# Performance work log

Measured on AMD Instinct MI355X. Metric: run time of the kernel, lower is better.

Reference implementation:

```python
import jax, jax.numpy as jnp
import numpy as np

B, N1, N2, D = 2, 500, 800, 128
THRESHOLD = 0.5

def setup_inputs() -> dict:
    key = jax.random.key(0)
    ks = jax.random.split(key, 7)
    return {
        "S_mol1": jax.random.randint(ks[0], (B, N1), 0, 21),
        "S_mol2": jax.random.randint(ks[1], (B, N2), 0, 21),
        "h_mol1": jax.random.normal(ks[2], (B, N1, D), jnp.float32),
        "h_mol2": jax.random.normal(ks[3], (B, N2, D), jnp.float32),
        "contact_map": jax.random.uniform(ks[4], (B, N1, N2), jnp.float32),
        "W1": jax.random.normal(ks[5], (2 * D, D), jnp.float32) / np.sqrt(2 * D).astype(np.float32),
        "b1": jnp.zeros((D,), jnp.float32),
        "W2": jax.random.normal(ks[6], (D, 1), jnp.float32) / np.sqrt(D).astype(np.float32),
        "b2": jnp.zeros((1,), jnp.float32),
    }

def reference(S_mol1, S_mol2, h_mol1, h_mol2, contact_map, W1, b1, W2, b2):
    m1 = (S_mol1 != 0).astype(jnp.float32)  # [B,N1]
    m2 = (S_mol2 != 0).astype(jnp.float32)  # [B,N2]
    # cat([h1_expand, h2_expand]) @ W1 == h1 @ W1[:D] + h2 @ W1[D:], broadcast over pairs
    p1 = jnp.einsum('bnd,df->bnf', h_mol1, W1[:D])   # [B,N1,D]
    p2 = jnp.einsum('bmd,df->bmf', h_mol2, W1[D:])   # [B,N2,D]
    hidden = jax.nn.relu(p1[:, :, None, :] + p2[:, None, :, :] + b1)  # [B,N1,N2,D]
    pred = (jnp.einsum('bnmd,do->bnmo', hidden, W2) + b2)[..., 0]     # [B,N1,N2]
    mask = m1[:, :, None] * m2[:, None, :]                             # [B,N1,N2]
    y_contact = (contact_map < THRESHOLD).astype(jnp.float32) * mask
    return (pred.reshape(B, -1), y_contact.reshape(B, -1), mask.reshape(B, -1))
```

## Files before the change

kernel.cpp:

```cpp
#include <hip/hip_runtime.h>

#define D_  128
#define B_  2
#define N1_ 500
#define N2_ 800

__global__ __launch_bounds__(256) void proj_kernel(
    const float* __restrict__ h1, const float* __restrict__ h2,
    const float* __restrict__ W1, const float* __restrict__ b1,
    float* __restrict__ P1, float* __restrict__ P2)
{
    __shared__ float hs[8][128];
    const int NB1 = (B_ * N1_ + 7) / 8;
    bool isP1 = (int)blockIdx.x < NB1;
    int r0 = (isP1 ? (int)blockIdx.x : (int)blockIdx.x - NB1) * 8;
    int R  = isP1 ? B_ * N1_ : B_ * N2_;
    const float* __restrict__ src = isP1 ? h1 : h2;
    float* __restrict__ dst = isP1 ? P1 : P2;
    const int koff = isP1 ? 0 : D_;

    int tid = threadIdx.x;
    {
        int row = tid >> 5;
        int c4  = (tid & 31) * 4;
        float4 v = make_float4(0.f, 0.f, 0.f, 0.f);
        int r = r0 + row;
        if (r < R) v = *reinterpret_cast<const float4*>(&src[(size_t)r * D_ + c4]);
        *reinterpret_cast<float4*>(&hs[row][c4]) = v;
    }
    __syncthreads();

    int c  = tid & 127;
    int rg = tid >> 7;
    const float* __restrict__ Wc = W1 + (size_t)koff * D_ + c;
    float acc[4];
    float binit = isP1 ? b1[c] : 0.f;
    #pragma unroll
    for (int i = 0; i < 4; ++i) acc[i] = binit;

    #pragma unroll 4
    for (int k4 = 0; k4 < D_; k4 += 4) {
        float w0 = Wc[(k4 + 0) * D_];
        float w1 = Wc[(k4 + 1) * D_];
        float w2 = Wc[(k4 + 2) * D_];
        float w3 = Wc[(k4 + 3) * D_];
        #pragma unroll
        for (int i = 0; i < 4; ++i) {
            float4 h = *reinterpret_cast<const float4*>(&hs[rg * 4 + i][k4]);
            acc[i] = fmaf(h.x, w0, acc[i]);
            acc[i] = fmaf(h.y, w1, acc[i]);
            acc[i] = fmaf(h.z, w2, acc[i]);
            acc[i] = fmaf(h.w, w3, acc[i]);
        }
    }
    #pragma unroll
    for (int i = 0; i < 4; ++i) {
        int r = r0 + rg * 4 + i;
        if (r < R) dst[(size_t)r * D_ + c] = acc[i];
    }
}

__global__ __launch_bounds__(256) void pair_kernel(
    const int* __restrict__ S1, const int* __restrict__ S2,
    const float* __restrict__ contact,
    const float* __restrict__ P1, const float* __restrict__ P2,
    const float* __restrict__ W2, const float* __restrict__ b2,
    float* __restrict__ out)
{
    const int NT = 16, MT = 128;
    const int nTn = (N1_ + NT - 1) / NT;
    const int nTm = (N2_ + MT - 1) / MT;
    int bid = blockIdx.x;
    int tb  = bid / (nTn * nTm);
    int rem = bid % (nTn * nTm);
    int tn  = rem / nTm;
    int tm  = rem % nTm;
    int n0 = tn * NT, m0 = tm * MT;
    int tid = threadIdx.x, lane = tid & 63, wave = tid >> 6;
    bool fullTile = (m0 + MT <= N2_);

    __shared__ float p2s[128 * 132];
    __shared__ float p1s[16 * 128];
    __shared__ float w2s[128];
    __shared__ float m1s[16];

    const float* __restrict__ P2b = P2 + ((size_t)tb * N2_ + m0) * D_;
    #pragma unroll
    for (int j = 0; j < 16; ++j) {
        int fi  = tid + j * 256;
        int row = fi >> 5;
        int c4  = (fi & 31) * 4;
        float4 v = make_float4(0.f, 0.f, 0.f, 0.f);
        if (m0 + row < N2_) v = *reinterpret_cast<const float4*>(&P2b[row * D_ + c4]);
        *reinterpret_cast<float4*>(&p2s[row * 132 + c4]) = v;
    }
    const float* __restrict__ P1b = P1 + ((size_t)tb * N1_ + n0) * D_;
    #pragma unroll
    for (int j = 0; j < 2; ++j) {
        int fi  = tid + j * 256;
        int row = fi >> 5;
        int c4  = (fi & 31) * 4;
        float4 v = make_float4(0.f, 0.f, 0.f, 0.f);
        if (n0 + row < N1_) v = *reinterpret_cast<const float4*>(&P1b[row * D_ + c4]);
        *reinterpret_cast<float4*>(&p1s[row * 128 + c4]) = v;
    }
    if (tid < 32)
        *reinterpret_cast<float4*>(&w2s[tid * 4]) =
            *reinterpret_cast<const float4*>(&W2[tid * 4]);
    if (tid >= 64 && tid < 80) {
        int i = tid - 64;
        m1s[i] = (n0 + i < N1_ && S1[tb * N1_ + n0 + i] != 0) ? 1.f : 0.f;
    }
    int mA = m0 + lane;
    int mB = m0 + 64 + lane;
    float m2A = (mA < N2_ && S2[tb * N2_ + mA] != 0) ? 1.f : 0.f;
    float m2B = (fullTile && S2[tb * N2_ + mB] != 0) ? 1.f : 0.f;
    float bias2 = b2[0];
    __syncthreads();

    int nw = wave * 4;
    float acc0[4] = {0.f, 0.f, 0.f, 0.f};
    float acc1[4] = {0.f, 0.f, 0.f, 0.f};
    const float* p2a = &p2s[lane * 132];
    const float* p2b = &p2s[(lane + 64) * 132];
    const float* p1p = &p1s[nw * 128];

    if (fullTile) {
        #pragma unroll 4
        for (int d = 0; d < D_; d += 4) {
            float4 qa = *reinterpret_cast<const float4*>(&p2a[d]);
            float4 qb = *reinterpret_cast<const float4*>(&p2b[d]);
            float4 w  = *reinterpret_cast<const float4*>(&w2s[d]);
            #pragma unroll
            for (int i = 0; i < 4; ++i) {
                float4 q1 = *reinterpret_cast<const float4*>(&p1p[i * 128 + d]);
                acc0[i] = fmaf(fmaxf(q1.x + qa.x, 0.f), w.x, acc0[i]);
                acc0[i] = fmaf(fmaxf(q1.y + qa.y, 0.f), w.y, acc0[i]);
                acc0[i] = fmaf(fmaxf(q1.z + qa.z, 0.f), w.z, acc0[i]);
                acc0[i] = fmaf(fmaxf(q1.w + qa.w, 0.f), w.w, acc0[i]);
                acc1[i] = fmaf(fmaxf(q1.x + qb.x, 0.f), w.x, acc1[i]);
                acc1[i] = fmaf(fmaxf(q1.y + qb.y, 0.f), w.y, acc1[i]);
                acc1[i] = fmaf(fmaxf(q1.z + qb.z, 0.f), w.z, acc1[i]);
                acc1[i] = fmaf(fmaxf(q1.w + qb.w, 0.f), w.w, acc1[i]);
            }
        }
    } else {
        #pragma unroll 4
        for (int d = 0; d < D_; d += 4) {
            float4 qa = *reinterpret_cast<const float4*>(&p2a[d]);
            float4 w  = *reinterpret_cast<const float4*>(&w2s[d]);
            #pragma unroll
            for (int i = 0; i < 4; ++i) {
                float4 q1 = *reinterpret_cast<const float4*>(&p1p[i * 128 + d]);
                acc0[i] = fmaf(fmaxf(q1.x + qa.x, 0.f), w.x, acc0[i]);
                acc0[i] = fmaf(fmaxf(q1.y + qa.y, 0.f), w.y, acc0[i]);
                acc0[i] = fmaf(fmaxf(q1.z + qa.z, 0.f), w.z, acc0[i]);
                acc0[i] = fmaf(fmaxf(q1.w + qa.w, 0.f), w.w, acc0[i]);
            }
        }
    }

    const size_t NN  = (size_t)N1_ * N2_;
    const size_t TOT = (size_t)B_ * NN;
    #pragma unroll
    for (int i = 0; i < 4; ++i) {
        int n = n0 + nw + i;
        if (n >= N1_) break;
        float m1v = m1s[nw + i];
        size_t rowoff = (size_t)tb * NN + (size_t)n * N2_;
        if (mA < N2_) {
            float mk = m1v * m2A;
            size_t off = rowoff + mA;
            float cv = contact[off];
            out[off]           = acc0[i] + bias2;
            out[TOT + off]     = (cv < 0.5f) ? mk : 0.f;
            out[2 * TOT + off] = mk;
        }
        if (fullTile) {
            float mk = m1v * m2B;
            size_t off = rowoff + mB;
            float cv = contact[off];
            out[off]           = acc1[i] + bias2;
            out[TOT + off]     = (cv < 0.5f) ? mk : 0.f;
            out[2 * TOT + off] = mk;
        }
    }
}

extern "C" void kernel_launch(void* const* d_in, const int* in_sizes, int n_in,
                              void* d_out, int out_size, void* d_ws, size_t ws_size,
                              hipStream_t stream) {
    const int*   S1      = (const int*)d_in[0];
    const int*   S2      = (const int*)d_in[1];
    const float* h1      = (const float*)d_in[2];
    const float* h2      = (const float*)d_in[3];
    const float* contact = (const float*)d_in[4];
    const float* W1      = (const float*)d_in[5];
    const float* b1      = (const float*)d_in[6];
    const float* W2      = (const float*)d_in[7];
    const float* b2      = (const float*)d_in[8];
    float* out = (float*)d_out;

    float* P1 = (float*)d_ws;
    float* P2 = P1 + (size_t)B_ * N1_ * D_;

    const int projBlocks = (B_ * N1_ + 7) / 8 + (B_ * N2_) / 8;
    proj_kernel<<<projBlocks, 256, 0, stream>>>(h1, h2, W1, b1, P1, P2);

    const int pairBlocks = B_ * ((N1_ + 15) / 16) * ((N2_ + 127) / 128);
    pair_kernel<<<pairBlocks, 256, 0, stream>>>(S1, S2, contact, P1, P2, W2, b2, out);
}
```

Measured before the change: 98.54 us.

## Prefetch contact and masks before compute; shrink projection tiles; read W2 directly

The projection kernel now handles 4 rows per block with 2 accumulators per thread, which doubles the block count and drops the bounds checks. In the pair kernel, the contact values and the S1 masks are loaded into registers before the compute loop, so their global latency overlaps with the shared-memory staging. The W2 and mask shared arrays are removed and W2 is read straight from global memory. Full tiles also skip bounds checks when staging P2. The catch is extra register pressure from the prefetched arrays, and more global loads of W2 inside the inner loop, which presumably hit cache.

```diff
diff --git a/kernel.cpp b/kernel.cpp
--- a/kernel.cpp
+++ b/kernel.cpp
@@ -10,54 +10,48 @@
     const float* __restrict__ W1, const float* __restrict__ b1,
     float* __restrict__ P1, float* __restrict__ P2)
 {
-    __shared__ float hs[8][128];
-    const int NB1 = (B_ * N1_ + 7) / 8;
+    __shared__ float hs[4][128];
+    const int NB1 = (B_ * N1_) / 4;
     bool isP1 = (int)blockIdx.x < NB1;
-    int r0 = (isP1 ? (int)blockIdx.x : (int)blockIdx.x - NB1) * 8;
-    int R  = isP1 ? B_ * N1_ : B_ * N2_;
+    int r0 = (isP1 ? (int)blockIdx.x : (int)blockIdx.x - NB1) * 4;
     const float* __restrict__ src = isP1 ? h1 : h2;
     float* __restrict__ dst = isP1 ? P1 : P2;
     const int koff = isP1 ? 0 : D_;
 
     int tid = threadIdx.x;
-    {
+    if (tid < 128) {
         int row = tid >> 5;
         int c4  = (tid & 31) * 4;
-        float4 v = make_float4(0.f, 0.f, 0.f, 0.f);
-        int r = r0 + row;
-        if (r < R) v = *reinterpret_cast<const float4*>(&src[(size_t)r * D_ + c4]);
-        *reinterpret_cast<float4*>(&hs[row][c4]) = v;
+        *reinterpret_cast<float4*>(&hs[row][c4]) =
+            *reinterpret_cast<const float4*>(&src[(size_t)(r0 + row) * D_ + c4]);
     }
     __syncthreads();
 
     int c  = tid & 127;
     int rg = tid >> 7;
     const float* __restrict__ Wc = W1 + (size_t)koff * D_ + c;
-    float acc[4];
     float binit = isP1 ? b1[c] : 0.f;
-    #pragma unroll
-    for (int i = 0; i < 4; ++i) acc[i] = binit;
-
-    #pragma unroll 4
+    float a0 = binit, a1 = binit;
+
+    #pragma unroll 8
     for (int k4 = 0; k4 < D_; k4 += 4) {
         float w0 = Wc[(k4 + 0) * D_];
         float w1 = Wc[(k4 + 1) * D_];
         float w2 = Wc[(k4 + 2) * D_];
         float w3 = Wc[(k4 + 3) * D_];
-        #pragma unroll
-        for (int i = 0; i < 4; ++i) {
-            float4 h = *reinterpret_cast<const float4*>(&hs[rg * 4 + i][k4]);
-            acc[i] = fmaf(h.x, w0, acc[i]);
-            acc[i] = fmaf(h.y, w1, acc[i]);
-            acc[i] = fmaf(h.z, w2, acc[i]);
-            acc[i] = fmaf(h.w, w3, acc[i]);
-        }
-    }
-    #pragma unroll
-    for (int i = 0; i < 4; ++i) {
-        int r = r0 + rg * 4 + i;
-        if (r < R) dst[(size_t)r * D_ + c] = acc[i];
-    }
+        float4 ha = *reinterpret_cast<const float4*>(&hs[rg * 2 + 0][k4]);
+        float4 hb = *reinterpret_cast<const float4*>(&hs[rg * 2 + 1][k4]);
+        a0 = fmaf(ha.x, w0, a0);
+        a0 = fmaf(ha.y, w1, a0);
+        a0 = fmaf(ha.z, w2, a0);
+        a0 = fmaf(ha.w, w3, a0);
+        a1 = fmaf(hb.x, w0, a1);
+        a1 = fmaf(hb.y, w1, a1);
+        a1 = fmaf(hb.z, w2, a1);
+        a1 = fmaf(hb.w, w3, a1);
+    }
+    dst[(size_t)(r0 + rg * 2 + 0) * D_ + c] = a0;
+    dst[(size_t)(r0 + rg * 2 + 1) * D_ + c] = a1;
 }
 
 __global__ __launch_bounds__(256) void pair_kernel(
@@ -81,18 +75,27 @@
 
     __shared__ float p2s[128 * 132];
     __shared__ float p1s[16 * 128];
-    __shared__ float w2s[128];
-    __shared__ float m1s[16];
 
     const float* __restrict__ P2b = P2 + ((size_t)tb * N2_ + m0) * D_;
-    #pragma unroll
-    for (int j = 0; j < 16; ++j) {
-        int fi  = tid + j * 256;
-        int row = fi >> 5;
-        int c4  = (fi & 31) * 4;
-        float4 v = make_float4(0.f, 0.f, 0.f, 0.f);
-        if (m0 + row < N2_) v = *reinterpret_cast<const float4*>(&P2b[row * D_ + c4]);
-        *reinterpret_cast<float4*>(&p2s[row * 132 + c4]) = v;
+    if (fullTile) {
+        #pragma unroll
+        for (int j = 0; j < 16; ++j) {
+            int fi  = tid + j * 256;
+            int row = fi >> 5;
+            int c4  = (fi & 31) * 4;
+            *reinterpret_cast<float4*>(&p2s[row * 132 + c4]) =
+                *reinterpret_cast<const float4*>(&P2b[row * D_ + c4]);
+        }
+    } else {
+        #pragma unroll
+        for (int j = 0; j < 16; ++j) {
+            int fi  = tid + j * 256;
+            int row = fi >> 5;
+            int c4  = (fi & 31) * 4;
+            float4 v = make_float4(0.f, 0.f, 0.f, 0.f);
+            if (m0 + row < N2_) v = *reinterpret_cast<const float4*>(&P2b[row * D_ + c4]);
+            *reinterpret_cast<float4*>(&p2s[row * 132 + c4]) = v;
+        }
     }
     const float* __restrict__ P1b = P1 + ((size_t)tb * N1_ + n0) * D_;
     #pragma unroll
@@ -104,21 +107,28 @@
         if (n0 + row < N1_) v = *reinterpret_cast<const float4*>(&P1b[row * D_ + c4]);
         *reinterpret_cast<float4*>(&p1s[row * 128 + c4]) = v;
     }
-    if (tid < 32)
-        *reinterpret_cast<float4*>(&w2s[tid * 4]) =
-            *reinterpret_cast<const float4*>(&W2[tid * 4]);
-    if (tid >= 64 && tid < 80) {
-        int i = tid - 64;
-        m1s[i] = (n0 + i < N1_ && S1[tb * N1_ + n0 + i] != 0) ? 1.f : 0.f;
-    }
+
+    int nw = wave * 4;
     int mA = m0 + lane;
     int mB = m0 + 64 + lane;
     float m2A = (mA < N2_ && S2[tb * N2_ + mA] != 0) ? 1.f : 0.f;
     float m2B = (fullTile && S2[tb * N2_ + mB] != 0) ? 1.f : 0.f;
     float bias2 = b2[0];
+
+    const size_t NN  = (size_t)N1_ * N2_;
+    const size_t TOT = (size_t)B_ * NN;
+    float m1v[4], cvA[4], cvB[4];
+    #pragma unroll
+    for (int i = 0; i < 4; ++i) {
+        int n = n0 + nw + i;
+        bool nok = (n < N1_);
+        m1v[i] = (nok && S1[tb * N1_ + n] != 0) ? 1.f : 0.f;
+        size_t rowoff = (size_t)tb * NN + (size_t)n * N2_;
+        cvA[i] = (nok && mA < N2_) ? contact[rowoff + mA] : 1.f;
+        cvB[i] = (nok && fullTile) ? contact[rowoff + mB] : 1.f;
+    }
     __syncthreads();
 
-    int nw = wave * 4;
     float acc0[4] = {0.f, 0.f, 0.f, 0.f};
     float acc1[4] = {0.f, 0.f, 0.f, 0.f};
     const float* p2a = &p2s[lane * 132];
@@ -130,7 +140,7 @@
         for (int d = 0; d < D_; d += 4) {
             float4 qa = *reinterpret_cast<const float4*>(&p2a[d]);
             float4 qb = *reinterpret_cast<const float4*>(&p2b[d]);
-            float4 w  = *reinterpret_cast<const float4*>(&w2s[d]);
+            float4 w  = *reinterpret_cast<const float4*>(&W2[d]);
             #pragma unroll
             for (int i = 0; i < 4; ++i) {
                 float4 q1 = *reinterpret_cast<const float4*>(&p1p[i * 128 + d]);
@@ -148,7 +158,7 @@
         #pragma unroll 4
         for (int d = 0; d < D_; d += 4) {
             float4 qa = *reinterpret_cast<const float4*>(&p2a[d]);
-            float4 w  = *reinterpret_cast<const float4*>(&w2s[d]);
+            float4 w  = *reinterpret_cast<const float4*>(&W2[d]);
             #pragma unroll
             for (int i = 0; i < 4; ++i) {
                 float4 q1 = *reinterpret_cast<const float4*>(&p1p[i * 128 + d]);
@@ -160,28 +170,24 @@
         }
     }
 
-    const size_t NN  = (size_t)N1_ * N2_;
-    const size_t TOT = (size_t)B_ * NN;
     #pragma unroll
     for (int i = 0; i < 4; ++i) {
         int n = n0 + nw + i;
         if (n >= N1_) break;
-        float m1v = m1s[nw + i];
+        float m1 = m1v[i];
         size_t rowoff = (size_t)tb * NN + (size_t)n * N2_;
         if (mA < N2_) {
-            float mk = m1v * m2A;
+            float mk = m1 * m2A;
             size_t off = rowoff + mA;
-            float cv = contact[off];
             out[off]           = acc0[i] + bias2;
-            out[TOT + off]     = (cv < 0.5f) ? mk : 0.f;
+            out[TOT + off]     = (cvA[i] < 0.5f) ? mk : 0.f;
             out[2 * TOT + off] = mk;
         }
         if (fullTile) {
-            float mk = m1v * m2B;
+            float mk = m1 * m2B;
             size_t off = rowoff + mB;
-            float cv = contact[off];
             out[off]           = acc1[i] + bias2;
-            out[TOT + off]     = (cv < 0.5f) ? mk : 0.f;
+            out[TOT + off]     = (cvB[i] < 0.5f) ? mk : 0.f;
             out[2 * TOT + off] = mk;
         }
     }
@@ -204,7 +210,7 @@
     float* P1 = (float*)d_ws;
     float* P2 = P1 + (size_t)B_ * N1_ * D_;
 
-    const int projBlocks = (B_ * N1_ + 7) / 8 + (B_ * N2_) / 8;
+    const int projBlocks = (B_ * N1_) / 4 + (B_ * N2_) / 4;
     proj_kernel<<<projBlocks, 256, 0, stream>>>(h1, h2, W1, b1, P1, P2);
 
     const int pairBlocks = B_ * ((N1_ + 15) / 16) * ((N2_ + 127) / 128);
```

Result: no change. 98.17 us (-0.4%).
